# Performance work log

Measured on AMD Instinct MI355X. Metric: run time of the kernel, lower is better.

## Reference

```python
import jax, jax.numpy as jnp
import numpy as np

L, Q = 256, 21
LAMBDA_H = 1e-06
LAMBDA_J = 0.0001
M = 8192


def setup_inputs() -> dict:
    key = jax.random.key(0)
    k1, k2, k3, k4 = jax.random.split(key, 4)
    seqs = jax.random.randint(k1, (M, L), 0, Q, dtype=jnp.int64 if jax.config.jax_enable_x64 else jnp.int32)
    weights = jax.random.uniform(k2, (M,), dtype=jnp.float32)
    h = jax.random.normal(k3, (L, Q), dtype=jnp.float32) * 0.1
    J = jax.random.normal(k4, (L, L, Q, Q), dtype=jnp.float32) * 0.02
    return {"seqs": seqs, "weights": weights, "h": h, "J": J}


def reference(seqs, weights, h, J):
    # strictly-lower-triangular mask over (i, j): j < i
    tril = jnp.tril(jnp.ones((L, L), dtype=bool), k=-1)
    Jm = J * tril[:, :, None, None]                       # (L, L, q, q)

    # one-hot history; H[b, j, k] = 1 iff seqs[b, j] == k
    H = jax.nn.one_hot(seqs, Q, dtype=h.dtype)            # (M, L, q)

    # contrib[b, i, a] = sum_{j<i, k} J[i, j, a, k] * H[b, j, k]
    # == one big (M, L*q) x (L*q, L*q) causal-masked matmul
    contrib = jnp.einsum('ijak,bjk->bia', Jm, H)          # (M, L, q)

    logits = h[None, :, :] + contrib                      # (M, L, q)
    logp = jax.nn.log_softmax(logits, axis=-1)            # (M, L, q)

    # gather label log-probs
    ll = jnp.take_along_axis(logp, seqs[..., None], axis=-1)[..., 0]  # (M, L)

    M_eff = jnp.maximum(weights.sum(), 1e-12)
    w_norm = weights / M_eff
    nll = -(w_norm[:, None] * ll).sum()

    reg_h = 0.5 * LAMBDA_H * jnp.sum(h ** 2)
    reg_J = 0.5 * LAMBDA_J * jnp.sum(Jm ** 2)
    loss = nll + reg_h + reg_J
    return (loss, nll, reg_h + reg_J)
```

## Files before the change

kernel.cpp:

```cpp
#include <hip/hip_runtime.h>
#include <cstdint>
#include <cstddef>

#define L_   256
#define Q_   21
#define M_   8192
#define QQ   441
#define JCH  16
#define SCALE    32.0f
#define INVSCALE 0.03125f
#define NPAIR ((L_ * (L_ - 1)) / 2)
#define PPB   16
#define PREPB (NPAIR / PPB)


typedef _Float16 h2 __attribute__((ext_vector_type(2)));

__device__ __forceinline__ float block_reduce_sum(float v) {
    __shared__ float s[256];
    int t = threadIdx.x;
    __syncthreads();
    s[t] = v;
    __syncthreads();
#pragma unroll
    for (int o = 128; o > 0; o >>= 1) {
        if (t < o) s[t] += s[t + o];
        __syncthreads();
    }
    return s[0];
}

__device__ __forceinline__ int tri_invert(int n) {
    int i = (int)((1.0f + sqrtf(8.0f * (float)n + 1.0f)) * 0.5f);
    while (i * (i - 1) / 2 > n) --i;
    while (i * (i - 1) / 2 + i <= n) ++i;
    return i;
}

__global__ __launch_bounds__(256) void k_prep(const float* __restrict__ J,
                                              unsigned* __restrict__ Jt,
                                              float* __restrict__ acc) {
    __shared__ float sB[PPB * QQ];
    const int t = threadIdx.x;
    const int n0 = blockIdx.x * PPB;

    float v2acc = 0.f;
#pragma unroll 1
    for (int p = 0; p < PPB; ++p) {
        const int n = n0 + p;
        const int i = tri_invert(n);
        const int j = n - i * (i - 1) / 2;
        const float* blk = J + ((size_t)i * L_ + j) * QQ;
        float* dst = sB + p * QQ;
        for (int x = t; x < QQ; x += 256) {
            float v = blk[x];
            dst[x] = v;
            v2acc += v * v;
        }
    }
    __syncthreads();

    {
        const int p = t >> 4;
        const int n = n0 + p;
        const int i = tri_invert(n);
        const int j = n - i * (i - 1) / 2;
        const size_t ij = (size_t)i * L_ + j;
        const float* s = sB + p * QQ;
#pragma unroll
        for (int u = 0; u < 16; ++u) {
            const int d = (t & 15) + (u << 4);
            const int kr = d / 12;
            const int dw = d - 12 * kr;
            const int a0 = dw * 2;
            unsigned outw = 0;
            if (kr < Q_) {
                float x0 = (a0 + 0 < Q_) ? s[(a0 + 0) * Q_ + kr] : 0.f;
                float x1 = (a0 + 1 < Q_) ? s[(a0 + 1) * Q_ + kr] : 0.f;
                union { _Float16 hh[2]; unsigned u; } uu;
                uu.hh[0] = (_Float16)(x0 * SCALE);
                uu.hh[1] = (_Float16)(x1 * SCALE);
                outw = uu.u;
            }
            Jt[ij * 256 + d] = outw;
        }
    }

    float r = block_reduce_sum(v2acc);
    if (t == 0) atomicAdd(&acc[4 + (blockIdx.x & 255)], r);
}

__global__ __launch_bounds__(256) void k_prep2(const int* __restrict__ seqs,
                                               const float* __restrict__ w,
                                               const float* __restrict__ h,
                                               unsigned* __restrict__ seqsP,
                                               float* __restrict__ acc) {
    const int bid = blockIdx.x;
    const int t = threadIdx.x;
    if (bid < 32) {
        const int b = bid * 256 + t;
        const int4* row = reinterpret_cast<const int4*>(seqs + (size_t)b * L_);
#pragma unroll 4
        for (int jq = 0; jq < L_ / 4; ++jq) {
            int4 v = row[jq];
            unsigned p = (unsigned)(v.x & 255) | ((unsigned)(v.y & 255) << 8) |
                         ((unsigned)(v.z & 255) << 16) | ((unsigned)(v.w & 255) << 24);
            seqsP[jq * M_ + b] = p;
        }
    } else {
        float v = 0.f;
        for (int x = t; x < M_; x += 256) v += w[x];
        float r = block_reduce_sum(v);
        if (t == 0) acc[0] = r;
        float v2 = 0.f;
        for (int x = t; x < L_ * Q_; x += 256) { float y = h[x]; v2 += y * y; }
        float r2 = block_reduce_sum(v2);
        if (t == 0) acc[2] = r2;
    }
}

#define BODY(jj)                                                                    \
    {                                                                               \
        const unsigned kk = (idxw[(jj) >> 2] >> (((jj) & 3) * 8)) & 255u;           \
        const uint4* rp = reinterpret_cast<const uint4*>(sJ) + ((jj) * 64 + kk * 3);\
        union { uint4 u; h2 h[4]; } ra, rb, rc;                                     \
        ra.u = rp[0]; rb.u = rp[1]; rc.u = rp[2];                                   \
        acch[0]  += ra.h[0]; acch[1]  += ra.h[1];                                   \
        acch[2]  += ra.h[2]; acch[3]  += ra.h[3];                                   \
        acch[4]  += rb.h[0]; acch[5]  += rb.h[1];                                   \
        acch[6]  += rb.h[2]; acch[7]  += rb.h[3];                                   \
        acch[8]  += rc.h[0]; acch[9]  += rc.h[1];                                   \
        acch[10] += rc.h[2]; acch[11] += rc.h[3];                                   \
    }

__global__ __launch_bounds__(256, 8) void k_main(const unsigned* __restrict__ Jt,
                                                 const float* __restrict__ h,
                                                 const unsigned* __restrict__ seqsP,
                                                 const float* __restrict__ weights,
                                                 float* __restrict__ acc) {
    __shared__ unsigned sJ[JCH * 256];

    const int bid = blockIdx.x;
    const int i = (L_ - 1) - (bid >> 5);
    const int b = ((bid & 31) << 8) + threadIdx.x;

    h2 acch[12];
    const float* hp = h + i * Q_;
#pragma unroll
    for (int m = 0; m < 10; ++m) {
        acch[m].x = (_Float16)(hp[2 * m] * SCALE);
        acch[m].y = (_Float16)(hp[2 * m + 1] * SCALE);
    }
    acch[10].x = (_Float16)(hp[20] * SCALE); acch[10].y = (_Float16)0.f;
    acch[11].x = (_Float16)0.f;              acch[11].y = (_Float16)0.f;

    const unsigned* Jrow = Jt + (size_t)i * (256 * 256);

    const int nStages = i >> 4;
    const int rem     = i & 15;

    for (int s = 0; s < nStages; ++s) {
        const int j0 = s << 4;
        {
            const uint4* src = reinterpret_cast<const uint4*>(Jrow + j0 * 256);
            uint4* dst = reinterpret_cast<uint4*>(sJ);
#pragma unroll
            for (int n = 0; n < 4; ++n) {
                dst[n * 256 + threadIdx.x] = src[n * 256 + threadIdx.x];
            }
        }
        __syncthreads();

        unsigned idxw[JCH / 4];
#pragma unroll
        for (int q = 0; q < JCH / 4; ++q) {
            idxw[q] = seqsP[((j0 >> 2) + q) * M_ + b];
        }

#pragma unroll
        for (int jj = 0; jj < JCH; ++jj) BODY(jj);

        __syncthreads();
    }

    if (rem) {
        const int j0 = nStages << 4;
        {
            const uint4* src = reinterpret_cast<const uint4*>(Jrow + j0 * 256);
            uint4* dst = reinterpret_cast<uint4*>(sJ);
#pragma unroll
            for (int n = 0; n < 4; ++n) {
                dst[n * 256 + threadIdx.x] = src[n * 256 + threadIdx.x];
            }
        }
        __syncthreads();

        unsigned idxw[JCH / 4];
#pragma unroll
        for (int q = 0; q < JCH / 4; ++q) {
            idxw[q] = seqsP[((j0 >> 2) + q) * M_ + b];
        }

#pragma unroll
        for (int jj = 0; jj < JCH; ++jj) {
            if (jj >= rem) break;
            BODY(jj);
        }
    }

    float l[21];
#pragma unroll
    for (int m = 0; m < 10; ++m) {
        l[2 * m]     = (float)acch[m].x * INVSCALE;
        l[2 * m + 1] = (float)acch[m].y * INVSCALE;
    }
    l[20] = (float)acch[10].x * INVSCALE;

    unsigned lw = seqsP[(i >> 2) * M_ + b];
    int lbl = (int)((lw >> ((i & 3) * 8)) & 255u);

    float m = l[0];
#pragma unroll
    for (int a = 1; a < 21; ++a) m = fmaxf(m, l[a]);
    float s = 0.f;
    float lv = l[0];
#pragma unroll
    for (int a = 0; a < 21; ++a) {
        s += __expf(l[a] - m);
        if (a > 0) lv = (a == lbl) ? l[a] : lv;
    }
    float ll = (lv - m) - __logf(s);
    float contrib = weights[b] * ll;

    float r = block_reduce_sum(contrib);
    if (threadIdx.x == 0) atomicAdd(&acc[260 + (bid & 127)], r);
}

__global__ void k_final(const float* __restrict__ acc, float* __restrict__ out) {
    int t = threadIdx.x;
    float j2p = acc[4 + t];
    float j2 = block_reduce_sum(j2p);
    float llp = (t < 128) ? acc[260 + t] : 0.f;
    float lls = block_reduce_sum(llp);
    if (t == 0) {
        float wsum = fmaxf(acc[0], 1e-12f);
        float nll = -lls / wsum;
        float reg = 0.5e-6f * acc[2] + 0.5e-4f * j2;
        out[0] = nll + reg;
        out[1] = nll;
        out[2] = reg;
    }
}

extern "C" void kernel_launch(void* const* d_in, const int* in_sizes, int n_in,
                              void* d_out, int out_size, void* d_ws, size_t ws_size,
                              hipStream_t stream) {
    const int*   seqs    = (const int*)d_in[0];
    const float* weights = (const float*)d_in[1];
    const float* h       = (const float*)d_in[2];
    const float* J       = (const float*)d_in[3];
    float* out = (float*)d_out;

    char* ws = (char*)d_ws;
    float*    acc   = (float*)ws;
    unsigned* seqsP = (unsigned*)(ws + 2048);
    unsigned* Jt    = (unsigned*)(ws + 2048 + (size_t)(L_ / 4) * M_ * sizeof(unsigned));

    hipMemsetAsync(d_ws, 0, 2048, stream);

    k_prep<<<PREPB, 256, 0, stream>>>(J, Jt, acc);
    k_prep2<<<33, 256, 0, stream>>>(seqs, weights, h, seqsP, acc);
    k_main<<<L_ * (M_ / 256), 256, 0, stream>>>(Jt, h, seqsP, weights, acc);
    k_final<<<1, 256, 0, stream>>>(acc, out);
}
```

Baseline: 417.9 us.

## Vectorize J prep with 2D row-chunk grid and widen seqs packing grid

The J preprocessing kernel now uses a 2D grid over (row i, 16-column chunk) instead of triangular index inversion. It loads each contiguous chunk of J with float4 loads and writes the transposed fp16 blocks as uint4 stores. The sequence packing kernel is split across 8x more blocks by column chunk, and the weight and h reductions now run in separate blocks. This targets low bandwidth use and poor parallelism in the prep kernels, at the cost of some idle blocks in the upper triangle.

Measured after the change: 391.9 us. -6.2%, faster.

```diff
diff --git a/kernel.cpp b/kernel.cpp
--- a/kernel.cpp
+++ b/kernel.cpp
@@ -10,8 +10,6 @@
 #define SCALE    32.0f
 #define INVSCALE 0.03125f
 #define NPAIR ((L_ * (L_ - 1)) / 2)
-#define PPB   16
-#define PREPB (NPAIR / PPB)
 
 
 typedef _Float16 h2 __attribute__((ext_vector_type(2)));
@@ -30,64 +28,69 @@
     return s[0];
 }
 
-__device__ __forceinline__ int tri_invert(int n) {
-    int i = (int)((1.0f + sqrtf(8.0f * (float)n + 1.0f)) * 0.5f);
-    while (i * (i - 1) / 2 > n) --i;
-    while (i * (i - 1) / 2 + i <= n) ++i;
-    return i;
-}
-
 __global__ __launch_bounds__(256) void k_prep(const float* __restrict__ J,
                                               unsigned* __restrict__ Jt,
                                               float* __restrict__ acc) {
-    __shared__ float sB[PPB * QQ];
-    const int t = threadIdx.x;
-    const int n0 = blockIdx.x * PPB;
-
-    float v2acc = 0.f;
-#pragma unroll 1
-    for (int p = 0; p < PPB; ++p) {
-        const int n = n0 + p;
-        const int i = tri_invert(n);
-        const int j = n - i * (i - 1) / 2;
-        const float* blk = J + ((size_t)i * L_ + j) * QQ;
-        float* dst = sB + p * QQ;
-        for (int x = t; x < QQ; x += 256) {
-            float v = blk[x];
-            dst[x] = v;
-            v2acc += v * v;
+    __shared__ __align__(16) float sB[16 * QQ];
+    const int t  = threadIdx.x;
+    const int i  = blockIdx.y + 1;
+    const int j0 = blockIdx.x << 4;
+    if (j0 >= i) return;
+    const int jn = min(16, i - j0);
+
+    const size_t base_dw = (size_t)(i * L_ + j0) * QQ;
+    const float* src = J + base_dw;
+    const int ndw = jn * QQ;
+    const int nf4 = ndw >> 2;
+    const int rem = ndw & 3;
+
+    float v2 = 0.f;
+    {
+        const float4* src4 = reinterpret_cast<const float4*>(src);
+        float4* s4 = reinterpret_cast<float4*>(sB);
+        for (int q = t; q < nf4; q += 256) {
+            float4 v = src4[q];
+            s4[q] = v;
+            v2 += v.x * v.x + v.y * v.y + v.z * v.z + v.w * v.w;
+        }
+        if (t < rem) {
+            float v = src[(nf4 << 2) + t];
+            sB[(nf4 << 2) + t] = v;
+            v2 += v * v;
         }
     }
     __syncthreads();
 
     {
-        const int p = t >> 4;
-        const int n = n0 + p;
-        const int i = tri_invert(n);
-        const int j = n - i * (i - 1) / 2;
-        const size_t ij = (size_t)i * L_ + j;
-        const float* s = sB + p * QQ;
-#pragma unroll
-        for (int u = 0; u < 16; ++u) {
-            const int d = (t & 15) + (u << 4);
-            const int kr = d / 12;
-            const int dw = d - 12 * kr;
-            const int a0 = dw * 2;
-            unsigned outw = 0;
-            if (kr < Q_) {
-                float x0 = (a0 + 0 < Q_) ? s[(a0 + 0) * Q_ + kr] : 0.f;
-                float x1 = (a0 + 1 < Q_) ? s[(a0 + 1) * Q_ + kr] : 0.f;
-                union { _Float16 hh[2]; unsigned u; } uu;
-                uu.hh[0] = (_Float16)(x0 * SCALE);
-                uu.hh[1] = (_Float16)(x1 * SCALE);
-                outw = uu.u;
+        const int nu4 = jn << 6;
+        uint4* dst = reinterpret_cast<uint4*>(Jt + (size_t)(i * L_ + j0) * 256);
+        for (int g = t; g < nu4; g += 256) {
+            const float* s = sB + (g >> 6) * QQ;
+            unsigned wv[4];
+#pragma unroll
+            for (int c = 0; c < 4; ++c) {
+                const int dd = ((g & 63) << 2) | c;
+                const int kr = dd / 12;
+                const int dw = dd - 12 * kr;
+                const int a0 = dw << 1;
+                unsigned outw = 0;
+                if (kr < Q_) {
+                    float x0 = (a0     < Q_) ? s[(a0    ) * Q_ + kr] : 0.f;
+                    float x1 = (a0 + 1 < Q_) ? s[(a0 + 1) * Q_ + kr] : 0.f;
+                    union { _Float16 hh[2]; unsigned u; } uu;
+                    uu.hh[0] = (_Float16)(x0 * SCALE);
+                    uu.hh[1] = (_Float16)(x1 * SCALE);
+                    outw = uu.u;
+                }
+                wv[c] = outw;
             }
-            Jt[ij * 256 + d] = outw;
-        }
-    }
-
-    float r = block_reduce_sum(v2acc);
-    if (t == 0) atomicAdd(&acc[4 + (blockIdx.x & 255)], r);
+            uint4 o; o.x = wv[0]; o.y = wv[1]; o.z = wv[2]; o.w = wv[3];
+            dst[g] = o;
+        }
+    }
+
+    float r = block_reduce_sum(v2);
+    if (t == 0) atomicAdd(&acc[4 + ((blockIdx.y * 16 + blockIdx.x) & 255)], r);
 }
 
 __global__ __launch_bounds__(256) void k_prep2(const int* __restrict__ seqs,
@@ -97,21 +100,25 @@
                                                float* __restrict__ acc) {
     const int bid = blockIdx.x;
     const int t = threadIdx.x;
-    if (bid < 32) {
-        const int b = bid * 256 + t;
+    if (bid < 256) {
+        const int bc = bid >> 3;
+        const int jc = bid & 7;
+        const int b = bc * 256 + t;
         const int4* row = reinterpret_cast<const int4*>(seqs + (size_t)b * L_);
-#pragma unroll 4
-        for (int jq = 0; jq < L_ / 4; ++jq) {
+#pragma unroll
+        for (int u = 0; u < 8; ++u) {
+            const int jq = jc * 8 + u;
             int4 v = row[jq];
             unsigned p = (unsigned)(v.x & 255) | ((unsigned)(v.y & 255) << 8) |
                          ((unsigned)(v.z & 255) << 16) | ((unsigned)(v.w & 255) << 24);
             seqsP[jq * M_ + b] = p;
         }
-    } else {
+    } else if (bid == 256) {
         float v = 0.f;
         for (int x = t; x < M_; x += 256) v += w[x];
         float r = block_reduce_sum(v);
         if (t == 0) acc[0] = r;
+    } else {
         float v2 = 0.f;
         for (int x = t; x < L_ * Q_; x += 256) { float y = h[x]; v2 += y * y; }
         float r2 = block_reduce_sum(v2);
@@ -268,8 +275,9 @@
 
     hipMemsetAsync(d_ws, 0, 2048, stream);
 
-    k_prep<<<PREPB, 256, 0, stream>>>(J, Jt, acc);
-    k_prep2<<<33, 256, 0, stream>>>(seqs, weights, h, seqsP, acc);
+    dim3 pg(16, 255);
+    k_prep<<<pg, 256, 0, stream>>>(J, Jt, acc);
+    k_prep2<<<258, 256, 0, stream>>>(seqs, weights, h, seqsP, acc);
     k_main<<<L_ * (M_ / 256), 256, 0, stream>>>(Jt, h, seqsP, weights, acc);
     k_final<<<1, 256, 0, stream>>>(acc, out);
 }
```
